# Optimization experiments

Measured on AMD Instinct MI355X. Metric: run time of the kernel, lower is better.

The kernel has to match this reference:

```python
import jax, jax.numpy as jnp
import numpy as np

D = 1024
H = 16
HD = D // H


def setup_inputs() -> dict:
    key = jax.random.key(0)
    ks = jax.random.split(key, 11)
    B, S = 4, 1024
    s = 0.02
    return {
        "q": jax.random.normal(ks[0], (B, S, D), jnp.float32),
        "k": jax.random.normal(ks[1], (B, S, D), jnp.float32),
        "v": jax.random.normal(ks[2], (B, S, D), jnp.float32),
        "Wq": jax.random.normal(ks[3], (D, D), jnp.float32) * s,
        "bq": jnp.zeros((D,), jnp.float32),
        "Wk": jax.random.normal(ks[4], (D, D), jnp.float32) * s,
        "bk": jnp.zeros((D,), jnp.float32),
        "Wv": jax.random.normal(ks[5], (D, D), jnp.float32) * s,
        "bv": jnp.zeros((D,), jnp.float32),
        "Wo": jax.random.normal(ks[6], (D, D), jnp.float32) * s,
        "bo": jnp.zeros((D,), jnp.float32),
    }


def _split_heads(x):
    # [B, S, D] -> [B, H, S, HD]
    B, S, _ = x.shape
    return x.reshape(B, S, H, HD).transpose(0, 2, 1, 3)


def reference(q, k, v, Wq, bq, Wk, bk, Wv, bv, Wo, bo):
    # Projections followed by ReLU (faithful to the original module)
    qh = _split_heads(jax.nn.relu(q @ Wq + bq))
    kh = _split_heads(jax.nn.relu(k @ Wk + bk))
    vh = _split_heads(jax.nn.relu(v @ Wv + bv))
    # NOTE: original scales by sqrt(input_dim), not sqrt(head_dim)
    scale = 1.0 / jnp.sqrt(jnp.float32(D))
    scores = jnp.einsum("bhsd,bhtd->bhst", qh, kh) * scale  # [B,H,S,S]
    weights = jax.nn.softmax(scores, axis=-1)  # dropout is identity in eval
    attn = jnp.einsum("bhst,bhtd->bhsd", weights, vh)  # [B,H,S,HD]
    B, _, S, _ = attn.shape
    attn = attn.transpose(0, 2, 1, 3).reshape(B, S, D)
    return attn @ Wo + bo
```

## Files before the change

### kernel.cpp

```cpp
#include <hip/hip_runtime.h>
#include <math.h>

#define Dm 1024
#define Hn 16
#define HDn 64
#define Sn 1024

typedef __attribute__((ext_vector_type(8))) __bf16 bf16x8;
typedef __attribute__((ext_vector_type(4))) float floatx4;

__device__ __forceinline__ void async_ld16(void* lds, const void* g) {
    __builtin_amdgcn_global_load_lds(
        (const __attribute__((address_space(1))) void*)g,
        (__attribute__((address_space(3))) void*)lds,
        16, 0, 0);
}

__global__ __launch_bounds__(256) void cast_qkv_kernel(
    const float* __restrict__ a, const float* __restrict__ b, const float* __restrict__ c,
    __bf16* __restrict__ oa, __bf16* __restrict__ ob, __bf16* __restrict__ oc)
{
    const int lin = blockIdx.x * 256 + threadIdx.x;
    const float* src = (blockIdx.y == 0) ? a : (blockIdx.y == 1) ? b : c;
    __bf16* dst = (blockIdx.y == 0) ? oa : (blockIdx.y == 1) ? ob : oc;
    const float4 v0 = ((const float4*)src)[lin * 2];
    const float4 v1 = ((const float4*)src)[lin * 2 + 1];
    bf16x8 o;
    o[0] = (__bf16)v0.x; o[1] = (__bf16)v0.y; o[2] = (__bf16)v0.z; o[3] = (__bf16)v0.w;
    o[4] = (__bf16)v1.x; o[5] = (__bf16)v1.y; o[6] = (__bf16)v1.z; o[7] = (__bf16)v1.w;
    ((bf16x8*)dst)[lin] = o;
}

__global__ __launch_bounds__(256) void cast_wt_kernel(
    const float* __restrict__ W0, const float* __restrict__ W1,
    const float* __restrict__ W2, const float* __restrict__ W3,
    __bf16* __restrict__ O0, __bf16* __restrict__ O1,
    __bf16* __restrict__ O2, __bf16* __restrict__ O3)
{
    __shared__ float sT[64][65];
    const int z = blockIdx.z;
    const float* W = (z == 0) ? W0 : (z == 1) ? W1 : (z == 2) ? W2 : W3;
    __bf16* O = (z == 0) ? O0 : (z == 1) ? O1 : (z == 2) ? O2 : O3;

    const int tid = threadIdx.x;
    const int bi = blockIdx.y * 64, bj = blockIdx.x * 64;
    const int colr = tid & 63, rowg = tid >> 6;

    #pragma unroll
    for (int i = 0; i < 16; ++i) {
        const int kk = i * 4 + rowg;
        sT[kk][colr] = W[(size_t)(bi + kk) * Dm + bj + colr];
    }
    __syncthreads();
    #pragma unroll
    for (int i = 0; i < 16; ++i) {
        const int rn = i * 4 + rowg;
        O[(size_t)(bj + rn) * Dm + bi + colr] = (__bf16)sT[colr][rn];
    }
}

__global__ __launch_bounds__(256) void gemm_bf16_kernel(
    const __bf16* __restrict__ Xb, const __bf16* __restrict__ WTb,
    const float* __restrict__ bias, void* __restrict__ outp,
    int layout, int do_relu, float escale)
{
    __shared__ __align__(16) __bf16 sA[128 * 32];
    __shared__ __align__(16) __bf16 sB[64 * 32];

    const int tid = threadIdx.x;
    const int bm = blockIdx.y * 128, bn = blockIdx.x * 64;
    const int lane = tid & 63;
    const int wave = tid >> 6;
    const int wm = (wave & 1) * 64;
    const int wn = (wave >> 1) * 32;
    const int l15 = lane & 15, quad = lane >> 4;

    floatx4 acc[4][2];
    #pragma unroll
    for (int mi = 0; mi < 4; ++mi)
        #pragma unroll
        for (int ni = 0; ni < 2; ++ni)
            acc[mi][ni] = (floatx4){0.f, 0.f, 0.f, 0.f};

    const int ciA0 = tid,       rA0 = ciA0 >> 2, qA0 = (ciA0 & 3) ^ (rA0 & 3);
    const int ciA1 = 256 + tid, rA1 = ciA1 >> 2, qA1 = (ciA1 & 3) ^ (rA1 & 3);
    const int rB = tid >> 2,    qB = (tid & 3) ^ (rB & 3);
    const __bf16* gA0 = Xb + (size_t)(bm + rA0) * Dm + qA0 * 8;
    const __bf16* gA1 = Xb + (size_t)(bm + rA1) * Dm + qA1 * 8;
    const __bf16* gB  = WTb + (size_t)(bn + rB) * Dm + qB * 8;
    char* lA0 = (char*)sA + (tid & 192) * 16;
    char* lA1 = (char*)sA + (256 + (tid & 192)) * 16;
    char* lB  = (char*)sB + (tid & 192) * 16;

    const __bf16* fA[4];
    const __bf16* fB[2];
    #pragma unroll
    for (int mi = 0; mi < 4; ++mi) {
        const int r = wm + mi * 16 + l15;
        fA[mi] = sA + r * 32 + ((quad ^ (r & 3)) * 8);
    }
    #pragma unroll
    for (int ni = 0; ni < 2; ++ni) {
        const int r = wn + ni * 16 + l15;
        fB[ni] = sB + r * 32 + ((quad ^ (r & 3)) * 8);
    }

    for (int kt = 0; kt < Dm; kt += 32) {
        async_ld16(lA0, gA0 + kt);
        async_ld16(lA1, gA1 + kt);
        async_ld16(lB,  gB  + kt);
        __syncthreads();

        bf16x8 af[4], bfr[2];
        #pragma unroll
        for (int mi = 0; mi < 4; ++mi) af[mi] = *(const bf16x8*)fA[mi];
        #pragma unroll
        for (int ni = 0; ni < 2; ++ni) bfr[ni] = *(const bf16x8*)fB[ni];
        #pragma unroll
        for (int mi = 0; mi < 4; ++mi)
            #pragma unroll
            for (int ni = 0; ni < 2; ++ni)
                acc[mi][ni] = __builtin_amdgcn_mfma_f32_16x16x32_bf16(
                    af[mi], bfr[ni], acc[mi][ni], 0, 0, 0);
        __syncthreads();
    }

    #pragma unroll
    for (int mi = 0; mi < 4; ++mi) {
        #pragma unroll
        for (int ni = 0; ni < 2; ++ni) {
            const int n = bn + wn + ni * 16 + l15;
            const float bv = bias[n];
            const int h = n >> 6, d = n & 63;
            #pragma unroll
            for (int reg = 0; reg < 4; ++reg) {
                const int m = bm + wm + mi * 16 + quad * 4 + reg;
                const int b = m >> 10, s = m & 1023;
                float v = acc[mi][ni][reg] + bv;
                if (do_relu) v = fmaxf(v, 0.0f);
                v *= escale;
                if (layout == 0)
                    ((__bf16*)outp)[((size_t)(b * Hn + h) * 1024 + s) * 64 + d] = (__bf16)v;
                else if (layout == 1)
                    ((__bf16*)outp)[((size_t)(b * Hn + h) * 64 + d) * 1024 + s] = (__bf16)v;
                else
                    ((float*)outp)[(size_t)m * 1024 + n] = v;
            }
        }
    }
}

__global__ __launch_bounds__(256, 2) void flash_attn_kernel(
    const __bf16* __restrict__ Qh,
    const __bf16* __restrict__ Kh,
    const __bf16* __restrict__ Vt,
    __bf16* __restrict__ ctx)
{
    __shared__ __align__(16) char sKV[2][16384];
    __shared__ __align__(16) __bf16 sP[4][32 * 64];

    const int tid = threadIdx.x;
    const int wave = tid >> 6, lane = tid & 63;
    const int l15 = lane & 15, quad = lane >> 4;
    const int b = blockIdx.z, h = blockIdx.y;
    const int bh = b * Hn + h;
    const int qb = blockIdx.x * 128 + wave * 32;

    bf16x8 aQ[2][2];
    #pragma unroll
    for (int mi = 0; mi < 2; ++mi)
        #pragma unroll
        for (int ks = 0; ks < 2; ++ks)
            aQ[mi][ks] = *(const bf16x8*)(Qh +
                (size_t)(bh * Sn + qb + mi * 16 + l15) * 64 + ks * 32 + quad * 8);

    const int s0 = tid, s1 = tid + 256;
    const int r0 = s0 >> 3, q0c = (s0 & 7) ^ (r0 & 7);
    const int r1 = s1 >> 3, q1c = (s1 & 7) ^ (r1 & 7);
    const __bf16* gK0 = Kh + (size_t)(bh * Sn + r0) * 64 + q0c * 8;
    const __bf16* gK1 = Kh + (size_t)(bh * Sn + r1) * 64 + q1c * 8;
    const __bf16* gV0 = Vt + (size_t)(bh * 64 + r0) * Sn + q0c * 8;
    const __bf16* gV1 = Vt + (size_t)(bh * 64 + r1) * Sn + q1c * 8;
    const int wofs = (tid & 192) * 16;

    floatx4 oacc[2][4];
    #pragma unroll
    for (int mi = 0; mi < 2; ++mi)
        #pragma unroll
        for (int nf = 0; nf < 4; ++nf)
            oacc[mi][nf] = (floatx4){0.f, 0.f, 0.f, 0.f};
    float lsum[2][4];
    #pragma unroll
    for (int mi = 0; mi < 2; ++mi)
        #pragma unroll
        for (int r = 0; r < 4; ++r) lsum[mi][r] = 0.0f;

    __bf16* sPw = sP[wave];

    {
        char* bK = sKV[0];
        char* bV = sKV[0] + 8192;
        async_ld16(bK + wofs,        gK0);
        async_ld16(bK + 4096 + wofs, gK1);
        async_ld16(bV + wofs,        gV0);
        async_ld16(bV + 4096 + wofs, gV1);
    }

    int cur = 0;
    for (int it = 0; it < 16; ++it) {
        __syncthreads();

        if (it + 1 < 16) {
            const int t0n = (it + 1) * 64;
            char* bK = sKV[cur ^ 1];
            char* bV = sKV[cur ^ 1] + 8192;
            async_ld16(bK + wofs,        gK0 + (size_t)t0n * 64);
            async_ld16(bK + 4096 + wofs, gK1 + (size_t)t0n * 64);
            async_ld16(bV + wofs,        gV0 + t0n);
            async_ld16(bV + 4096 + wofs, gV1 + t0n);
        }

        const __bf16* sK = (const __bf16*)sKV[cur];
        const __bf16* sV = (const __bf16*)(sKV[cur] + 8192);

        floatx4 sc[2][4];
        #pragma unroll
        for (int mi = 0; mi < 2; ++mi)
            #pragma unroll
            for (int nf = 0; nf < 4; ++nf)
                sc[mi][nf] = (floatx4){0.f, 0.f, 0.f, 0.f};
        #pragma unroll
        for (int ks = 0; ks < 2; ++ks) {
            bf16x8 bK[4];
            #pragma unroll
            for (int nf = 0; nf < 4; ++nf) {
                const int n = nf * 16 + l15;
                bK[nf] = *(const bf16x8*)(sK + (n * 8 + (((ks << 2) + quad) ^ (n & 7))) * 8);
            }
            #pragma unroll
            for (int mi = 0; mi < 2; ++mi)
                #pragma unroll
                for (int nf = 0; nf < 4; ++nf)
                    sc[mi][nf] = __builtin_amdgcn_mfma_f32_16x16x32_bf16(
                        aQ[mi][ks], bK[nf], sc[mi][nf], 0, 0, 0);
        }

        #pragma unroll
        for (int mi = 0; mi < 2; ++mi)
            #pragma unroll
            for (int nf = 0; nf < 4; ++nf) {
                const int t = nf * 16 + l15;
                #pragma unroll
                for (int r = 0; r < 4; ++r) {
                    const float p = __builtin_amdgcn_exp2f(fminf(sc[mi][nf][r], 126.0f));
                    const __bf16 pb = (__bf16)p;
                    lsum[mi][r] += (float)pb;
                    const int rr = mi * 16 + quad * 4 + r;
                    sPw[(rr * 8 + ((t >> 3) ^ (rr & 7))) * 8 + (t & 7)] = pb;
                }
            }

        #pragma unroll
        for (int ks = 0; ks < 2; ++ks) {
            bf16x8 aP[2], bV[4];
            #pragma unroll
            for (int mi = 0; mi < 2; ++mi) {
                const int r = mi * 16 + l15;
                aP[mi] = *(const bf16x8*)(sPw + (r * 8 + (((ks << 2) + quad) ^ (r & 7))) * 8);
            }
            #pragma unroll
            for (int nf = 0; nf < 4; ++nf) {
                const int n = nf * 16 + l15;
                bV[nf] = *(const bf16x8*)(sV + (n * 8 + (((ks << 2) + quad) ^ (n & 7))) * 8);
            }
            #pragma unroll
            for (int mi = 0; mi < 2; ++mi)
                #pragma unroll
                for (int nf = 0; nf < 4; ++nf)
                    oacc[mi][nf] = __builtin_amdgcn_mfma_f32_16x16x32_bf16(
                        aP[mi], bV[nf], oacc[mi][nf], 0, 0, 0);
        }

        cur ^= 1;
    }

    float linv[2][4];
    #pragma unroll
    for (int mi = 0; mi < 2; ++mi)
        #pragma unroll
        for (int r = 0; r < 4; ++r) {
            float l = lsum[mi][r];
            l += __shfl_xor(l, 1, 64);
            l += __shfl_xor(l, 2, 64);
            l += __shfl_xor(l, 4, 64);
            l += __shfl_xor(l, 8, 64);
            linv[mi][r] = 1.0f / l;
        }

    #pragma unroll
    for (int mi = 0; mi < 2; ++mi)
        #pragma unroll
        for (int nf = 0; nf < 4; ++nf) {
            const int d = h * 64 + nf * 16 + l15;
            #pragma unroll
            for (int reg = 0; reg < 4; ++reg) {
                const int s = qb + mi * 16 + quad * 4 + reg;
                ctx[(size_t)(b * Sn + s) * Dm + d] =
                    (__bf16)(oacc[mi][nf][reg] * linv[mi][reg]);
            }
        }
}

extern "C" void kernel_launch(void* const* d_in, const int* in_sizes, int n_in,
                              void* d_out, int out_size, void* d_ws, size_t ws_size,
                              hipStream_t stream)
{
    const float* q  = (const float*)d_in[0];
    const float* k  = (const float*)d_in[1];
    const float* v  = (const float*)d_in[2];
    const float* Wq = (const float*)d_in[3];
    const float* bq = (const float*)d_in[4];
    const float* Wk = (const float*)d_in[5];
    const float* bk = (const float*)d_in[6];
    const float* Wv = (const float*)d_in[7];
    const float* bv = (const float*)d_in[8];
    const float* Wo = (const float*)d_in[9];
    const float* bo = (const float*)d_in[10];

    char* ws = (char*)d_ws;
    const size_t MB = 1024 * 1024;
    __bf16* qb_ = (__bf16*)(ws);
    __bf16* kb_ = (__bf16*)(ws + 8 * MB);
    __bf16* vb_ = (__bf16*)(ws + 16 * MB);
    __bf16* WTq = (__bf16*)(ws + 24 * MB);
    __bf16* WTk = (__bf16*)(ws + 26 * MB);
    __bf16* WTv = (__bf16*)(ws + 28 * MB);
    __bf16* WTo = (__bf16*)(ws + 30 * MB);
    __bf16* Qh  = (__bf16*)(ws + 32 * MB);
    __bf16* Kh  = (__bf16*)(ws + 40 * MB);
    __bf16* Vt  = (__bf16*)(ws + 48 * MB);
    __bf16* ctx = (__bf16*)(ws + 56 * MB);

    cast_qkv_kernel<<<dim3(2048, 3), 256, 0, stream>>>(q, k, v, qb_, kb_, vb_);
    cast_wt_kernel<<<dim3(16, 16, 4), 256, 0, stream>>>(Wq, Wk, Wv, Wo,
                                                        WTq, WTk, WTv, WTo);

    const float QSCALE = 0.0450842200f;
    const dim3 gg(16, 32), tb(256);
    gemm_bf16_kernel<<<gg, tb, 0, stream>>>(qb_, WTq, bq, Qh, 0, 1, QSCALE);
    gemm_bf16_kernel<<<gg, tb, 0, stream>>>(kb_, WTk, bk, Kh, 0, 1, 1.0f);
    gemm_bf16_kernel<<<gg, tb, 0, stream>>>(vb_, WTv, bv, Vt, 1, 1, 1.0f);

    flash_attn_kernel<<<dim3(8, Hn, 4), 256, 0, stream>>>(Qh, Kh, Vt, ctx);

    gemm_bf16_kernel<<<gg, tb, 0, stream>>>(ctx, WTo, bo, d_out, 3, 0, 1.0f);
}
```

Measured before the change: 247.8 us.

## Widen GEMM tile to 128x128 and batch QKV projections into one launch

The GEMM block tile grows from 128x64 to 128x128, so each wave computes a 64x64 sub-tile with 4x4 MFMA accumulators. This raises arithmetic intensity and cuts redundant loads of the activation tile. The three Q/K/V projection launches are merged into one grid that uses blockIdx.z to select per-projection pointers and epilogue settings from a struct argument. In exchange the kernel uses more registers and LDS, which may lower occupancy, and the output projection now has fewer blocks.

```diff
diff --git a/kernel.cpp b/kernel.cpp
--- a/kernel.cpp
+++ b/kernel.cpp
@@ -59,48 +59,65 @@
     }
 }
 
-__global__ __launch_bounds__(256) void gemm_bf16_kernel(
-    const __bf16* __restrict__ Xb, const __bf16* __restrict__ WTb,
-    const float* __restrict__ bias, void* __restrict__ outp,
-    int layout, int do_relu, float escale)
+struct GemmArgs {
+    const __bf16* X[3];
+    const __bf16* WT[3];
+    const float*  bias[3];
+    void*         out[3];
+    int   layout[3];
+    int   relu[3];
+    float esc[3];
+};
+
+__global__ __launch_bounds__(256) void gemm_bf16_kernel(GemmArgs args)
 {
     __shared__ __align__(16) __bf16 sA[128 * 32];
-    __shared__ __align__(16) __bf16 sB[64 * 32];
+    __shared__ __align__(16) __bf16 sB[128 * 32];
+
+    const int z = blockIdx.z;
+    const __bf16* __restrict__ Xb  = args.X[z];
+    const __bf16* __restrict__ WTb = args.WT[z];
+    const float*  __restrict__ bias = args.bias[z];
+    void* __restrict__ outp = args.out[z];
+    const int layout = args.layout[z];
+    const int do_relu = args.relu[z];
+    const float escale = args.esc[z];
 
     const int tid = threadIdx.x;
-    const int bm = blockIdx.y * 128, bn = blockIdx.x * 64;
+    const int bm = blockIdx.y * 128, bn = blockIdx.x * 128;
     const int lane = tid & 63;
     const int wave = tid >> 6;
     const int wm = (wave & 1) * 64;
-    const int wn = (wave >> 1) * 32;
+    const int wn = (wave >> 1) * 64;
     const int l15 = lane & 15, quad = lane >> 4;
 
-    floatx4 acc[4][2];
+    floatx4 acc[4][4];
     #pragma unroll
     for (int mi = 0; mi < 4; ++mi)
         #pragma unroll
-        for (int ni = 0; ni < 2; ++ni)
+        for (int ni = 0; ni < 4; ++ni)
             acc[mi][ni] = (floatx4){0.f, 0.f, 0.f, 0.f};
 
-    const int ciA0 = tid,       rA0 = ciA0 >> 2, qA0 = (ciA0 & 3) ^ (rA0 & 3);
-    const int ciA1 = 256 + tid, rA1 = ciA1 >> 2, qA1 = (ciA1 & 3) ^ (rA1 & 3);
-    const int rB = tid >> 2,    qB = (tid & 3) ^ (rB & 3);
-    const __bf16* gA0 = Xb + (size_t)(bm + rA0) * Dm + qA0 * 8;
-    const __bf16* gA1 = Xb + (size_t)(bm + rA1) * Dm + qA1 * 8;
-    const __bf16* gB  = WTb + (size_t)(bn + rB) * Dm + qB * 8;
+    const int c0 = tid,       r0 = c0 >> 2, q0 = (c0 & 3) ^ (r0 & 3);
+    const int c1 = tid + 256, r1 = c1 >> 2, q1 = (c1 & 3) ^ (r1 & 3);
+    const __bf16* gA0 = Xb  + (size_t)(bm + r0) * Dm + q0 * 8;
+    const __bf16* gA1 = Xb  + (size_t)(bm + r1) * Dm + q1 * 8;
+    const __bf16* gB0 = WTb + (size_t)(bn + r0) * Dm + q0 * 8;
+    const __bf16* gB1 = WTb + (size_t)(bn + r1) * Dm + q1 * 8;
     char* lA0 = (char*)sA + (tid & 192) * 16;
     char* lA1 = (char*)sA + (256 + (tid & 192)) * 16;
-    char* lB  = (char*)sB + (tid & 192) * 16;
+    char* lB0 = (char*)sB + (tid & 192) * 16;
+    char* lB1 = (char*)sB + (256 + (tid & 192)) * 16;
 
     const __bf16* fA[4];
-    const __bf16* fB[2];
+    const __bf16* fB[4];
     #pragma unroll
     for (int mi = 0; mi < 4; ++mi) {
         const int r = wm + mi * 16 + l15;
         fA[mi] = sA + r * 32 + ((quad ^ (r & 3)) * 8);
     }
     #pragma unroll
-    for (int ni = 0; ni < 2; ++ni) {
+    for (int ni = 0; ni < 4; ++ni) {
         const int r = wn + ni * 16 + l15;
         fB[ni] = sB + r * 32 + ((quad ^ (r & 3)) * 8);
     }
@@ -108,18 +125,19 @@
     for (int kt = 0; kt < Dm; kt += 32) {
         async_ld16(lA0, gA0 + kt);
         async_ld16(lA1, gA1 + kt);
-        async_ld16(lB,  gB  + kt);
+        async_ld16(lB0, gB0 + kt);
+        async_ld16(lB1, gB1 + kt);
         __syncthreads();
 
-        bf16x8 af[4], bfr[2];
+        bf16x8 af[4], bfr[4];
         #pragma unroll
         for (int mi = 0; mi < 4; ++mi) af[mi] = *(const bf16x8*)fA[mi];
         #pragma unroll
-        for (int ni = 0; ni < 2; ++ni) bfr[ni] = *(const bf16x8*)fB[ni];
+        for (int ni = 0; ni < 4; ++ni) bfr[ni] = *(const bf16x8*)fB[ni];
         #pragma unroll
         for (int mi = 0; mi < 4; ++mi)
             #pragma unroll
-            for (int ni = 0; ni < 2; ++ni)
+            for (int ni = 0; ni < 4; ++ni)
                 acc[mi][ni] = __builtin_amdgcn_mfma_f32_16x16x32_bf16(
                     af[mi], bfr[ni], acc[mi][ni], 0, 0, 0);
         __syncthreads();
@@ -128,7 +146,7 @@
     #pragma unroll
     for (int mi = 0; mi < 4; ++mi) {
         #pragma unroll
-        for (int ni = 0; ni < 2; ++ni) {
+        for (int ni = 0; ni < 4; ++ni) {
             const int n = bn + wn + ni * 16 + l15;
             const float bv = bias[n];
             const int h = n >> 6, d = n & 63;
@@ -346,12 +364,26 @@
                                                         WTq, WTk, WTv, WTo);
 
     const float QSCALE = 0.0450842200f;
-    const dim3 gg(16, 32), tb(256);
-    gemm_bf16_kernel<<<gg, tb, 0, stream>>>(qb_, WTq, bq, Qh, 0, 1, QSCALE);
-    gemm_bf16_kernel<<<gg, tb, 0, stream>>>(kb_, WTk, bk, Kh, 0, 1, 1.0f);
-    gemm_bf16_kernel<<<gg, tb, 0, stream>>>(vb_, WTv, bv, Vt, 1, 1, 1.0f);
+
+    GemmArgs qkv;
+    qkv.X[0] = qb_;  qkv.X[1] = kb_;  qkv.X[2] = vb_;
+    qkv.WT[0] = WTq; qkv.WT[1] = WTk; qkv.WT[2] = WTv;
+    qkv.bias[0] = bq; qkv.bias[1] = bk; qkv.bias[2] = bv;
+    qkv.out[0] = Qh;  qkv.out[1] = Kh;  qkv.out[2] = Vt;
+    qkv.layout[0] = 0; qkv.layout[1] = 0; qkv.layout[2] = 1;
+    qkv.relu[0] = 1;   qkv.relu[1] = 1;   qkv.relu[2] = 1;
+    qkv.esc[0] = QSCALE; qkv.esc[1] = 1.0f; qkv.esc[2] = 1.0f;
+    gemm_bf16_kernel<<<dim3(8, 32, 3), 256, 0, stream>>>(qkv);
 
     flash_attn_kernel<<<dim3(8, Hn, 4), 256, 0, stream>>>(Qh, Kh, Vt, ctx);
 
-    gemm_bf16_kernel<<<gg, tb, 0, stream>>>(ctx, WTo, bo, d_out, 3, 0, 1.0f);
-}
+    GemmArgs og;
+    og.X[0] = ctx;  og.X[1] = ctx;  og.X[2] = ctx;
+    og.WT[0] = WTo; og.WT[1] = WTo; og.WT[2] = WTo;
+    og.bias[0] = bo; og.bias[1] = bo; og.bias[2] = bo;
+    og.out[0] = d_out; og.out[1] = d_out; og.out[2] = d_out;
+    og.layout[0] = 3; og.layout[1] = 3; og.layout[2] = 3;
+    og.relu[0] = 0;   og.relu[1] = 0;   og.relu[2] = 0;
+    og.esc[0] = 1.0f; og.esc[1] = 1.0f; og.esc[2] = 1.0f;
+    gemm_bf16_kernel<<<dim3(8, 32, 1), 256, 0, stream>>>(og);
+}
```

New measurement: 229.7 us. 1.08x faster.
